# Optimization experiments

Hardware: AMD Instinct MI355X
Metric: run time of the kernel (lower is better)

## Reference

```python
import jax, jax.numpy as jnp
import numpy as np

B, O, D = 64, 36, 512
G1, G2 = 512, 512  # interactor sizes
F1, F2 = 512, 512  # aggregator sizes
BN_EPS = 1e-5


def setup_inputs() -> dict:
    key = jax.random.key(0)
    ks = jax.random.split(key, 10)
    sc = 0.02
    return {
        "objs": jax.random.normal(ks[0], (B, O, D), jnp.float32),
        "W1": jax.random.normal(ks[1], (G1, 2 * D), jnp.float32) * sc,
        "b1": jax.random.normal(ks[2], (G1,), jnp.float32) * sc,
        "W2": jax.random.normal(ks[3], (G2, G1), jnp.float32) * sc,
        "b2": jax.random.normal(ks[4], (G2,), jnp.float32) * sc,
        "gamma": jnp.ones((G2,), jnp.float32),
        "beta": jnp.zeros((G2,), jnp.float32),
        "W3": jax.random.normal(ks[5], (F1, G2), jnp.float32) * sc,
        "b3": jax.random.normal(ks[6], (F1,), jnp.float32) * sc,
        "W4": jax.random.normal(ks[7], (F2, F1), jnp.float32) * sc,
        "b4": jax.random.normal(ks[8], (F2,), jnp.float32) * sc,
    }


def reference(objs, W1, b1, W2, b2, gamma, beta, W3, b3, W4, b4):
    b, o, d = objs.shape
    # make_pairs: x_full[b,k,m] = concat(v[b,m], v[b,k]) -> (b, o*o, 2d)
    v_i = jnp.broadcast_to(objs[:, None, :, :], (b, o, o, d))  # varies over m
    v_j = jnp.broadcast_to(objs[:, :, None, :], (b, o, o, d))  # varies over k
    pairs = jnp.concatenate([v_i, v_j], axis=-1).reshape(b, o * o, 2 * d)
    # interaction MLP g
    h = jax.nn.relu(jnp.einsum('bpc,gc->bpg', pairs, W1) + b1)
    x_pairs = jax.nn.relu(jnp.einsum('bpg,hg->bph', h, W2) + b2)
    # sum over pairs, BatchNorm1d (training mode: batch stats, biased var)
    s = x_pairs.sum(axis=1)  # (b, G2)
    mean = s.mean(axis=0)
    var = ((s - mean) ** 2).mean(axis=0)
    sn = (s - mean) / jnp.sqrt(var + BN_EPS) * gamma + beta
    # aggregation MLP f
    a = jax.nn.relu(sn @ W3.T + b3)
    agg = jax.nn.relu(a @ W4.T + b4)
    return agg, x_pairs
```

## Files before the change

### kernel.cpp

```cpp
#include <hip/hip_runtime.h>
#include <cstdint>
#include <cstddef>

#define B_  64
#define O_  36
#define D_  512
#define P_  (O_*O_)
#define BO_ (B_*O_)

typedef short s8v __attribute__((ext_vector_type(8)));
typedef float f4v __attribute__((ext_vector_type(4)));

__device__ __forceinline__ void bsplit(float x, short& hi, short& lo) {
    unsigned u = __float_as_uint(x);
    unsigned r = (u + 0x7FFFu + ((u >> 16) & 1u)) >> 16;
    hi = (short)r;
    float hf = __uint_as_float(r << 16);
    float d = x - hf;
    unsigned u2 = __float_as_uint(d);
    unsigned r2 = (u2 + 0x7FFFu + ((u2 >> 16) & 1u)) >> 16;
    lo = (short)r2;
}

__global__ __launch_bounds__(256) void wsplit_all(
    const float* __restrict__ W2, const float* __restrict__ W1,
    short* __restrict__ W2h, short* __restrict__ W2l,
    short* __restrict__ W1h, short* __restrict__ W1l)
{
    int i = (blockIdx.x * 256 + threadIdx.x) * 4;
    float4 w;
    short* hip_; short* lop_; int o;
    if (i < 512 * 512) {
        w = *(const float4*)&W2[i];
        hip_ = W2h; lop_ = W2l; o = i;
    } else {
        o = i - 512 * 512;
        const int n = o >> 9, d = o & 511;
        w = *(const float4*)&W1[(size_t)(n & 511) * 1024 + ((n >> 9) << 9) + d];
        hip_ = W1h; lop_ = W1l;
    }
    short h0, l0, h1, l1, h2, l2, h3, l3;
    bsplit(w.x, h0, l0); bsplit(w.y, h1, l1);
    bsplit(w.z, h2, l2); bsplit(w.w, h3, l3);
    *(short4*)&hip_[o] = make_short4(h0, h1, h2, h3);
    *(short4*)&lop_[o] = make_short4(l0, l1, l2, l3);
}

__global__ __launch_bounds__(256, 2) void uv_mfma(
    const float* __restrict__ objs,
    const short* __restrict__ W1h, const short* __restrict__ W1l,
    float* __restrict__ U, float* __restrict__ V)
{
    __shared__ short Ah[128 * 40];
    __shared__ short Al[128 * 40];
    __shared__ short Bh[128 * 40];
    __shared__ short Bl[128 * 40];

    const int tid  = threadIdx.x;
    const int lane = tid & 63;
    const int wid  = tid >> 6;
    const int wr   = wid >> 1, wc = wid & 1;
    const int rowbase = blockIdx.y * 128;
    const int colbase = blockIdx.x * 128;

    const int srow = tid >> 1;
    const int skq  = (tid & 1) * 8;
    const float* Xrow  = objs + (size_t)(rowbase + srow) * 512;
    const short* Whrow = W1h + (size_t)(colbase + srow) * 512;
    const short* Wlrow = W1l + (size_t)(colbase + srow) * 512;

    const int fr = lane & 15;
    const int sl = (lane >> 4) * 8;
    const int abase = (wr * 64 + fr) * 40 + sl;
    const int bbase = (wc * 64 + fr) * 40 + sl;

    f4v acc[4][4];
    const f4v zero = {0.f, 0.f, 0.f, 0.f};
    #pragma unroll
    for (int i = 0; i < 4; ++i)
        #pragma unroll
        for (int j = 0; j < 4; ++j) acc[i][j] = zero;

    for (int kt = 0; kt < 512; kt += 32) {
        __syncthreads();
        #pragma unroll
        for (int pass = 0; pass < 2; ++pass) {
            const int kq = skq + pass * 16;
            const float4 x0 = *(const float4*)&Xrow[kt + kq];
            const float4 x1 = *(const float4*)&Xrow[kt + kq + 4];
            float hx[8] = {x0.x, x0.y, x0.z, x0.w, x1.x, x1.y, x1.z, x1.w};
            s8v hi8, lo8;
            #pragma unroll
            for (int j = 0; j < 8; ++j) { short h, l; bsplit(hx[j], h, l); hi8[j] = h; lo8[j] = l; }
            *(s8v*)&Ah[srow * 40 + kq] = hi8;
            *(s8v*)&Al[srow * 40 + kq] = lo8;
            *(s8v*)&Bh[srow * 40 + kq] = *(const s8v*)&Whrow[kt + kq];
            *(s8v*)&Bl[srow * 40 + kq] = *(const s8v*)&Wlrow[kt + kq];
        }
        __syncthreads();

        s8v ah[4], al[4], bh[4], bl[4];
        #pragma unroll
        for (int f = 0; f < 4; ++f) {
            ah[f] = *(const s8v*)&Ah[abase + f * 640];
            al[f] = *(const s8v*)&Al[abase + f * 640];
            bh[f] = *(const s8v*)&Bh[bbase + f * 640];
            bl[f] = *(const s8v*)&Bl[bbase + f * 640];
        }
        #pragma unroll
        for (int fm = 0; fm < 4; ++fm)
            #pragma unroll
            for (int fn = 0; fn < 4; ++fn)
                acc[fm][fn] = __builtin_amdgcn_mfma_f32_16x16x32_bf16(ah[fm], bh[fn], acc[fm][fn], 0, 0, 0);
        #pragma unroll
        for (int fm = 0; fm < 4; ++fm)
            #pragma unroll
            for (int fn = 0; fn < 4; ++fn)
                acc[fm][fn] = __builtin_amdgcn_mfma_f32_16x16x32_bf16(ah[fm], bl[fn], acc[fm][fn], 0, 0, 0);
        #pragma unroll
        for (int fm = 0; fm < 4; ++fm)
            #pragma unroll
            for (int fn = 0; fn < 4; ++fn)
                acc[fm][fn] = __builtin_amdgcn_mfma_f32_16x16x32_bf16(al[fm], bh[fn], acc[fm][fn], 0, 0, 0);
    }

    float* dst = (colbase < 512) ? U : V;
    const int cb = colbase & 511;
    const int r4 = (lane >> 4) * 4;
    #pragma unroll
    for (int fm = 0; fm < 4; ++fm) {
        #pragma unroll
        for (int r = 0; r < 4; ++r) {
            const int row = rowbase + wr * 64 + fm * 16 + r4 + r;
            float* drow = &dst[(size_t)row * 512 + cb + wc * 64 + fr];
            #pragma unroll
            for (int fn = 0; fn < 4; ++fn) drow[fn * 16] = acc[fm][fn][r];
        }
    }
}

__global__ __launch_bounds__(256, 3) void pair_gemm(
    const float* __restrict__ U, const float* __restrict__ V,
    const float* __restrict__ b1,
    const short* __restrict__ W2h, const short* __restrict__ W2l,
    const float* __restrict__ b2,
    float* __restrict__ xout, float* __restrict__ s)
{
    __shared__ short Ah[4][128][8];
    __shared__ short Al[4][128][8];
    __shared__ short Bh[4][128][8];
    __shared__ short Bl[4][128][8];
    __shared__ float b1s[512];

    const int tid  = threadIdx.x;
    const int lane = tid & 63;
    const int wid  = tid >> 6;
    const int wr   = wid >> 1, wc = wid & 1;
    const int b       = blockIdx.z;
    const int pbase   = blockIdx.y * 128;
    const int colbase = blockIdx.x * 128;

    for (int g = tid; g < 512; g += 256) b1s[g] = b1[g];

    const int arow = tid & 127;
    const int a0   = (tid >> 7) * 2;
    const int p    = pbase + arow;
    const bool valid = (p < P_);
    int ki = 0, mi = 0;
    if (valid) { ki = p / O_; mi = p - ki * O_; }
    const float* Urow = U + (size_t)(b * O_ + mi) * 512;
    const float* Vrow = V + (size_t)(b * O_ + ki) * 512;

    const int boct = wid;
    const int brow = lane;
    const short* Wh0 = W2h + (size_t)(colbase + brow) * 512 + boct * 8;
    const short* Wh1 = Wh0 + (size_t)64 * 512;
    const short* Wl0 = W2l + (size_t)(colbase + brow) * 512 + boct * 8;
    const short* Wl1 = Wl0 + (size_t)64 * 512;

    const int fr = lane & 15;
    const int q  = lane >> 4;

    f4v acc[4][4];
    const f4v zero = {0.f, 0.f, 0.f, 0.f};
    #pragma unroll
    for (int i = 0; i < 4; ++i)
        #pragma unroll
        for (int j = 0; j < 4; ++j) acc[i][j] = zero;

    for (int kt = 0; kt < 512; kt += 32) {
        __syncthreads();
        const s8v wh0 = *(const s8v*)&Wh0[kt];
        const s8v wh1 = *(const s8v*)&Wh1[kt];
        const s8v wl0 = *(const s8v*)&Wl0[kt];
        const s8v wl1 = *(const s8v*)&Wl1[kt];
        #pragma unroll
        for (int j = 0; j < 2; ++j) {
            const int oct = a0 + j;
            const int k0  = kt + oct * 8;
            s8v hi8, lo8;
            if (valid) {
                const float4 u0 = *(const float4*)&Urow[k0];
                const float4 u1 = *(const float4*)&Urow[k0 + 4];
                const float4 v0 = *(const float4*)&Vrow[k0];
                const float4 v1 = *(const float4*)&Vrow[k0 + 4];
                const float4 c0 = *(const float4*)&b1s[k0];
                const float4 c1 = *(const float4*)&b1s[k0 + 4];
                float hx[8];
                hx[0] = fmaxf(u0.x + v0.x + c0.x, 0.f);
                hx[1] = fmaxf(u0.y + v0.y + c0.y, 0.f);
                hx[2] = fmaxf(u0.z + v0.z + c0.z, 0.f);
                hx[3] = fmaxf(u0.w + v0.w + c0.w, 0.f);
                hx[4] = fmaxf(u1.x + v1.x + c1.x, 0.f);
                hx[5] = fmaxf(u1.y + v1.y + c1.y, 0.f);
                hx[6] = fmaxf(u1.z + v1.z + c1.z, 0.f);
                hx[7] = fmaxf(u1.w + v1.w + c1.w, 0.f);
                #pragma unroll
                for (int e = 0; e < 8; ++e) { short h, l; bsplit(hx[e], h, l); hi8[e] = h; lo8[e] = l; }
            } else {
                #pragma unroll
                for (int e = 0; e < 8; ++e) { hi8[e] = 0; lo8[e] = 0; }
            }
            *(s8v*)&Ah[oct][arow][0] = hi8;
            *(s8v*)&Al[oct][arow][0] = lo8;
        }
        *(s8v*)&Bh[boct][brow][0]      = wh0;
        *(s8v*)&Bh[boct][64 + brow][0] = wh1;
        *(s8v*)&Bl[boct][brow][0]      = wl0;
        *(s8v*)&Bl[boct][64 + brow][0] = wl1;
        __syncthreads();

        s8v ah[4], al[4], bh[4], bl[4];
        #pragma unroll
        for (int f = 0; f < 4; ++f) {
            ah[f] = *(const s8v*)&Ah[q][wr * 64 + f * 16 + fr][0];
            al[f] = *(const s8v*)&Al[q][wr * 64 + f * 16 + fr][0];
            bh[f] = *(const s8v*)&Bh[q][wc * 64 + f * 16 + fr][0];
            bl[f] = *(const s8v*)&Bl[q][wc * 64 + f * 16 + fr][0];
        }
        #pragma unroll
        for (int fm = 0; fm < 4; ++fm)
            #pragma unroll
            for (int fn = 0; fn < 4; ++fn)
                acc[fm][fn] = __builtin_amdgcn_mfma_f32_16x16x32_bf16(ah[fm], bh[fn], acc[fm][fn], 0, 0, 0);
        #pragma unroll
        for (int fm = 0; fm < 4; ++fm)
            #pragma unroll
            for (int fn = 0; fn < 4; ++fn)
                acc[fm][fn] = __builtin_amdgcn_mfma_f32_16x16x32_bf16(ah[fm], bl[fn], acc[fm][fn], 0, 0, 0);
        #pragma unroll
        for (int fm = 0; fm < 4; ++fm)
            #pragma unroll
            for (int fn = 0; fn < 4; ++fn)
                acc[fm][fn] = __builtin_amdgcn_mfma_f32_16x16x32_bf16(al[fm], bh[fn], acc[fm][fn], 0, 0, 0);
    }

    float b2v[4];
    #pragma unroll
    for (int fn = 0; fn < 4; ++fn) b2v[fn] = b2[colbase + wc * 64 + fn * 16 + fr];
    const int r4 = (lane >> 4) * 4;
    float csum[4] = {0.f, 0.f, 0.f, 0.f};
    #pragma unroll
    for (int fm = 0; fm < 4; ++fm) {
        const int prow0 = pbase + wr * 64 + fm * 16 + r4;
        #pragma unroll
        for (int r = 0; r < 4; ++r) {
            const int pp = prow0 + r;
            if (pp < P_) {
                float* xrow = &xout[(size_t)(b * P_ + pp) * 512 + colbase + wc * 64 + fr];
                #pragma unroll
                for (int fn = 0; fn < 4; ++fn) {
                    float x = fmaxf(acc[fm][fn][r] + b2v[fn], 0.f);
                    xrow[fn * 16] = x;
                    csum[fn] += x;
                }
            }
        }
    }
    #pragma unroll
    for (int fn = 0; fn < 4; ++fn) {
        csum[fn] += __shfl_xor(csum[fn], 16);
        csum[fn] += __shfl_xor(csum[fn], 32);
    }
    if (lane < 16) {
        #pragma unroll
        for (int fn = 0; fn < 4; ++fn)
            atomicAdd(&s[b * 512 + colbase + wc * 64 + fn * 16 + lane], csum[fn]);
    }
}

__global__ __launch_bounds__(512) void bn_kernel(
    const float* __restrict__ s, const float* __restrict__ gamma,
    const float* __restrict__ beta, float* __restrict__ sn)
{
    const int g = threadIdx.x;
    float mean = 0.f;
    for (int b = 0; b < B_; ++b) mean += s[b * 512 + g];
    mean *= (1.f / B_);
    float var = 0.f;
    for (int b = 0; b < B_; ++b) { const float d = s[b * 512 + g] - mean; var = fmaf(d, d, var); }
    var *= (1.f / B_);
    const float inv = 1.f / sqrtf(var + 1e-5f);
    const float ga = gamma[g], be = beta[g];
    for (int b = 0; b < B_; ++b)
        sn[b * 512 + g] = (s[b * 512 + g] - mean) * inv * ga + be;
}

__global__ __launch_bounds__(256) void mlp512(
    const float* __restrict__ x, const float* __restrict__ W,
    const float* __restrict__ bias, float* __restrict__ out)
{
    __shared__ float xs[512];
    const int b = blockIdx.y;
    const int f = blockIdx.x * 256 + threadIdx.x;
    for (int g = threadIdx.x; g < 512; g += 256) xs[g] = x[b * 512 + g];
    __syncthreads();
    float sum = 0.f;
    #pragma unroll 8
    for (int k = 0; k < 512; k += 4) {
        const float4 w4 = *(const float4*)&W[(size_t)f * 512 + k];
        const float4 x4 = *(const float4*)&xs[k];
        sum = fmaf(w4.x, x4.x, sum); sum = fmaf(w4.y, x4.y, sum);
        sum = fmaf(w4.z, x4.z, sum); sum = fmaf(w4.w, x4.w, sum);
    }
    out[b * 512 + f] = fmaxf(sum + bias[f], 0.f);
}

extern "C" void kernel_launch(void* const* d_in, const int* in_sizes, int n_in,
                              void* d_out, int out_size, void* d_ws, size_t ws_size,
                              hipStream_t stream)
{
    const float* objs  = (const float*)d_in[0];
    const float* W1    = (const float*)d_in[1];
    const float* b1    = (const float*)d_in[2];
    const float* W2    = (const float*)d_in[3];
    const float* b2    = (const float*)d_in[4];
    const float* gamma = (const float*)d_in[5];
    const float* beta  = (const float*)d_in[6];
    const float* W3    = (const float*)d_in[7];
    const float* b3    = (const float*)d_in[8];
    const float* W4    = (const float*)d_in[9];
    const float* b4    = (const float*)d_in[10];

    float* out  = (float*)d_out;
    float* xout = out + B_ * 512;

    float* U  = (float*)d_ws;
    float* V  = U  + (size_t)BO_ * 512;
    float* s  = V  + (size_t)BO_ * 512;
    float* sn = s  + B_ * 512;
    float* a  = sn + B_ * 512;
    short* W2h = (short*)(a + B_ * 512);
    short* W2l = W2h + (size_t)512 * 512;
    short* W1h = W2l + (size_t)512 * 512;
    short* W1l = W1h + (size_t)1024 * 512;

    wsplit_all<<<768, 256, 0, stream>>>(W2, W1, W2h, W2l, W1h, W1l);
    uv_mfma<<<dim3(8, 18), 256, 0, stream>>>(objs, W1h, W1l, U, V);
    hipMemsetAsync(s, 0, B_ * 512 * sizeof(float), stream);
    pair_gemm<<<dim3(4, 11, B_), 256, 0, stream>>>(U, V, b1, W2h, W2l, b2, xout, s);
    bn_kernel<<<1, 512, 0, stream>>>(s, gamma, beta, sn);
    mlp512<<<dim3(2, B_), 256, 0, stream>>>(sn, W3, b3, a);
    mlp512<<<dim3(2, B_), 256, 0, stream>>>(a, W4, b4, out);
}
```

Before: 451.3 us.

## Double-buffer pair GEMM, load W2 fragments directly, fuse MLPs and memset

```diff
diff --git a/kernel.cpp b/kernel.cpp
--- a/kernel.cpp
+++ b/kernel.cpp
@@ -25,9 +25,13 @@
 __global__ __launch_bounds__(256) void wsplit_all(
     const float* __restrict__ W2, const float* __restrict__ W1,
     short* __restrict__ W2h, short* __restrict__ W2l,
-    short* __restrict__ W1h, short* __restrict__ W1l)
-{
-    int i = (blockIdx.x * 256 + threadIdx.x) * 4;
+    short* __restrict__ W1h, short* __restrict__ W1l,
+    float* __restrict__ s)
+{
+    const int gt = blockIdx.x * 256 + threadIdx.x;
+    if (gt < 8192)
+        *(float4*)&s[gt * 4] = make_float4(0.f, 0.f, 0.f, 0.f);
+    int i = gt * 4;
     float4 w;
     short* hip_; short* lop_; int o;
     if (i < 512 * 512) {
@@ -139,17 +143,15 @@
     }
 }
 
-__global__ __launch_bounds__(256, 3) void pair_gemm(
+__global__ __launch_bounds__(256, 2) void pair_gemm(
     const float* __restrict__ U, const float* __restrict__ V,
     const float* __restrict__ b1,
     const short* __restrict__ W2h, const short* __restrict__ W2l,
     const float* __restrict__ b2,
     float* __restrict__ xout, float* __restrict__ s)
 {
-    __shared__ short Ah[4][128][8];
-    __shared__ short Al[4][128][8];
-    __shared__ short Bh[4][128][8];
-    __shared__ short Bl[4][128][8];
+    __shared__ short Ah[2][4][128][8];
+    __shared__ short Al[2][4][128][8];
     __shared__ float b1s[512];
 
     const int tid  = threadIdx.x;
@@ -171,16 +173,70 @@
     const float* Urow = U + (size_t)(b * O_ + mi) * 512;
     const float* Vrow = V + (size_t)(b * O_ + ki) * 512;
 
-    const int boct = wid;
-    const int brow = lane;
-    const short* Wh0 = W2h + (size_t)(colbase + brow) * 512 + boct * 8;
-    const short* Wh1 = Wh0 + (size_t)64 * 512;
-    const short* Wl0 = W2l + (size_t)(colbase + brow) * 512 + boct * 8;
-    const short* Wl1 = Wl0 + (size_t)64 * 512;
-
     const int fr = lane & 15;
     const int q  = lane >> 4;
 
+    const short* Bhp[4]; const short* Blp[4];
+    #pragma unroll
+    for (int f = 0; f < 4; ++f) {
+        const size_t off = (size_t)(colbase + wc * 64 + f * 16 + fr) * 512 + q * 8;
+        Bhp[f] = W2h + off; Blp[f] = W2l + off;
+    }
+
+    float4 au0[2], au1[2], av0[2], av1[2];
+    s8v bhA[4], blA[4], bhB[4], blB[4];
+    s8v ah[4], al[4];
+
+#define LOAD_A(ktv) do { if (valid) { const int _k = (ktv); \
+    _Pragma("unroll") for (int _j = 0; _j < 2; ++_j) { \
+        const int _o = _k + (a0 + _j) * 8; \
+        au0[_j] = *(const float4*)&Urow[_o]; au1[_j] = *(const float4*)&Urow[_o + 4]; \
+        av0[_j] = *(const float4*)&Vrow[_o]; av1[_j] = *(const float4*)&Vrow[_o + 4]; } } } while (0)
+
+#define BUILD_WRITE(bufi, ktv) do { const int _k = (ktv); \
+    _Pragma("unroll") for (int _j = 0; _j < 2; ++_j) { \
+        const int _oct = a0 + _j; \
+        s8v _hi, _lo; \
+        if (valid) { \
+            const float4 _c0 = *(const float4*)&b1s[_k + _oct * 8]; \
+            const float4 _c1 = *(const float4*)&b1s[_k + _oct * 8 + 4]; \
+            float _hx[8]; \
+            _hx[0] = fmaxf(au0[_j].x + av0[_j].x + _c0.x, 0.f); \
+            _hx[1] = fmaxf(au0[_j].y + av0[_j].y + _c0.y, 0.f); \
+            _hx[2] = fmaxf(au0[_j].z + av0[_j].z + _c0.z, 0.f); \
+            _hx[3] = fmaxf(au0[_j].w + av0[_j].w + _c0.w, 0.f); \
+            _hx[4] = fmaxf(au1[_j].x + av1[_j].x + _c1.x, 0.f); \
+            _hx[5] = fmaxf(au1[_j].y + av1[_j].y + _c1.y, 0.f); \
+            _hx[6] = fmaxf(au1[_j].z + av1[_j].z + _c1.z, 0.f); \
+            _hx[7] = fmaxf(au1[_j].w + av1[_j].w + _c1.w, 0.f); \
+            _Pragma("unroll") for (int _e = 0; _e < 8; ++_e) { short _h, _l; bsplit(_hx[_e], _h, _l); _hi[_e] = _h; _lo[_e] = _l; } \
+        } else { \
+            _Pragma("unroll") for (int _e = 0; _e < 8; ++_e) { _hi[_e] = 0; _lo[_e] = 0; } \
+        } \
+        *(s8v*)&Ah[bufi][_oct][arow][0] = _hi; \
+        *(s8v*)&Al[bufi][_oct][arow][0] = _lo; } } while (0)
+
+#define LOAD_B(ktv, BH, BL) do { const int _k = (ktv); \
+    _Pragma("unroll") for (int _f = 0; _f < 4; ++_f) { \
+        BH[_f] = *(const s8v*)&Bhp[_f][_k]; BL[_f] = *(const s8v*)&Blp[_f][_k]; } } while (0)
+
+#define READ_FRAGS(bufi) do { \
+    _Pragma("unroll") for (int _f = 0; _f < 4; ++_f) { \
+        ah[_f] = *(const s8v*)&Ah[bufi][q][wr * 64 + _f * 16 + fr][0]; \
+        al[_f] = *(const s8v*)&Al[bufi][q][wr * 64 + _f * 16 + fr][0]; } } while (0)
+
+#define MFMA_STEP(BH, BL) do { \
+    _Pragma("unroll") for (int _fm = 0; _fm < 4; ++_fm) \
+        _Pragma("unroll") for (int _fn = 0; _fn < 4; ++_fn) \
+            acc[_fm][_fn] = __builtin_amdgcn_mfma_f32_16x16x32_bf16(ah[_fm], BH[_fn], acc[_fm][_fn], 0, 0, 0); \
+    _Pragma("unroll") for (int _fm = 0; _fm < 4; ++_fm) \
+        _Pragma("unroll") for (int _fn = 0; _fn < 4; ++_fn) \
+            acc[_fm][_fn] = __builtin_amdgcn_mfma_f32_16x16x32_bf16(ah[_fm], BL[_fn], acc[_fm][_fn], 0, 0, 0); \
+    _Pragma("unroll") for (int _fm = 0; _fm < 4; ++_fm) \
+        _Pragma("unroll") for (int _fn = 0; _fn < 4; ++_fn) \
+            acc[_fm][_fn] = __builtin_amdgcn_mfma_f32_16x16x32_bf16(al[_fm], BH[_fn], acc[_fm][_fn], 0, 0, 0); \
+    } while (0)
+
     f4v acc[4][4];
     const f4v zero = {0.f, 0.f, 0.f, 0.f};
     #pragma unroll
@@ -188,71 +244,28 @@
         #pragma unroll
         for (int j = 0; j < 4; ++j) acc[i][j] = zero;
 
-    for (int kt = 0; kt < 512; kt += 32) {
+    LOAD_A(0);
+    __syncthreads();
+    BUILD_WRITE(0, 0);
+    LOAD_A(32);
+    LOAD_B(0, bhA, blA);
+
+    for (int it = 0; it < 8; ++it) {
+        const int kt0 = it * 64;
         __syncthreads();
-        const s8v wh0 = *(const s8v*)&Wh0[kt];
-        const s8v wh1 = *(const s8v*)&Wh1[kt];
-        const s8v wl0 = *(const s8v*)&Wl0[kt];
-        const s8v wl1 = *(const s8v*)&Wl1[kt];
-        #pragma unroll
-        for (int j = 0; j < 2; ++j) {
-            const int oct = a0 + j;
-            const int k0  = kt + oct * 8;
-            s8v hi8, lo8;
-            if (valid) {
-                const float4 u0 = *(const float4*)&Urow[k0];
-                const float4 u1 = *(const float4*)&Urow[k0 + 4];
-                const float4 v0 = *(const float4*)&Vrow[k0];
-                const float4 v1 = *(const float4*)&Vrow[k0 + 4];
-                const float4 c0 = *(const float4*)&b1s[k0];
-                const float4 c1 = *(const float4*)&b1s[k0 + 4];
-                float hx[8];
-                hx[0] = fmaxf(u0.x + v0.x + c0.x, 0.f);
-                hx[1] = fmaxf(u0.y + v0.y + c0.y, 0.f);
-                hx[2] = fmaxf(u0.z + v0.z + c0.z, 0.f);
-                hx[3] = fmaxf(u0.w + v0.w + c0.w, 0.f);
-                hx[4] = fmaxf(u1.x + v1.x + c1.x, 0.f);
-                hx[5] = fmaxf(u1.y + v1.y + c1.y, 0.f);
-                hx[6] = fmaxf(u1.z + v1.z + c1.z, 0.f);
-                hx[7] = fmaxf(u1.w + v1.w + c1.w, 0.f);
-                #pragma unroll
-                for (int e = 0; e < 8; ++e) { short h, l; bsplit(hx[e], h, l); hi8[e] = h; lo8[e] = l; }
-            } else {
-                #pragma unroll
-                for (int e = 0; e < 8; ++e) { hi8[e] = 0; lo8[e] = 0; }
-            }
-            *(s8v*)&Ah[oct][arow][0] = hi8;
-            *(s8v*)&Al[oct][arow][0] = lo8;
-        }
-        *(s8v*)&Bh[boct][brow][0]      = wh0;
-        *(s8v*)&Bh[boct][64 + brow][0] = wh1;
-        *(s8v*)&Bl[boct][brow][0]      = wl0;
-        *(s8v*)&Bl[boct][64 + brow][0] = wl1;
+        READ_FRAGS(0);
+        LOAD_B(kt0 + 32, bhB, blB);
+        MFMA_STEP(bhA, blA);
+        BUILD_WRITE(1, kt0 + 32);
+        LOAD_A(kt0 + 64 > 480 ? 480 : kt0 + 64);
         __syncthreads();
-
-        s8v ah[4], al[4], bh[4], bl[4];
-        #pragma unroll
-        for (int f = 0; f < 4; ++f) {
-            ah[f] = *(const s8v*)&Ah[q][wr * 64 + f * 16 + fr][0];
-            al[f] = *(const s8v*)&Al[q][wr * 64 + f * 16 + fr][0];
-            bh[f] = *(const s8v*)&Bh[q][wc * 64 + f * 16 + fr][0];
-            bl[f] = *(const s8v*)&Bl[q][wc * 64 + f * 16 + fr][0];
-        }
-        #pragma unroll
-        for (int fm = 0; fm < 4; ++fm)
-            #pragma unroll
-            for (int fn = 0; fn < 4; ++fn)
-                acc[fm][fn] = __builtin_amdgcn_mfma_f32_16x16x32_bf16(ah[fm], bh[fn], acc[fm][fn], 0, 0, 0);
-        #pragma unroll
-        for (int fm = 0; fm < 4; ++fm)
-            #pragma unroll
-            for (int fn = 0; fn < 4; ++fn)
-                acc[fm][fn] = __builtin_amdgcn_mfma_f32_16x16x32_bf16(ah[fm], bl[fn], acc[fm][fn], 0, 0, 0);
-        #pragma unroll
-        for (int fm = 0; fm < 4; ++fm)
-            #pragma unroll
-            for (int fn = 0; fn < 4; ++fn)
-                acc[fm][fn] = __builtin_amdgcn_mfma_f32_16x16x32_bf16(al[fm], bh[fn], acc[fm][fn], 0, 0, 0);
+        READ_FRAGS(1);
+        LOAD_B(kt0 + 64 > 480 ? 480 : kt0 + 64, bhA, blA);
+        MFMA_STEP(bhB, blB);
+        if (it < 7) {
+            BUILD_WRITE(0, kt0 + 64);
+            LOAD_A(kt0 + 96 > 480 ? 480 : kt0 + 96);
+        }
     }
 
     float b2v[4];
@@ -287,6 +300,11 @@
         for (int fn = 0; fn < 4; ++fn)
             atomicAdd(&s[b * 512 + colbase + wc * 64 + fn * 16 + lane], csum[fn]);
     }
+#undef LOAD_A
+#undef BUILD_WRITE
+#undef LOAD_B
+#undef READ_FRAGS
+#undef MFMA_STEP
 }
 
 __global__ __launch_bounds__(512) void bn_kernel(
@@ -294,36 +312,55 @@
     const float* __restrict__ beta, float* __restrict__ sn)
 {
     const int g = threadIdx.x;
+    float v[64];
+    #pragma unroll
+    for (int b = 0; b < 64; ++b) v[b] = s[b * 512 + g];
     float mean = 0.f;
-    for (int b = 0; b < B_; ++b) mean += s[b * 512 + g];
+    #pragma unroll
+    for (int b = 0; b < 64; ++b) mean += v[b];
     mean *= (1.f / B_);
     float var = 0.f;
-    for (int b = 0; b < B_; ++b) { const float d = s[b * 512 + g] - mean; var = fmaf(d, d, var); }
+    #pragma unroll
+    for (int b = 0; b < 64; ++b) { const float d = v[b] - mean; var = fmaf(d, d, var); }
     var *= (1.f / B_);
     const float inv = 1.f / sqrtf(var + 1e-5f);
     const float ga = gamma[g], be = beta[g];
-    for (int b = 0; b < B_; ++b)
-        sn[b * 512 + g] = (s[b * 512 + g] - mean) * inv * ga + be;
-}
-
-__global__ __launch_bounds__(256) void mlp512(
-    const float* __restrict__ x, const float* __restrict__ W,
-    const float* __restrict__ bias, float* __restrict__ out)
+    #pragma unroll
+    for (int b = 0; b < 64; ++b)
+        sn[b * 512 + g] = (v[b] - mean) * inv * ga + be;
+}
+
+__global__ __launch_bounds__(512) void mlp_fused(
+    const float* __restrict__ sn,
+    const float* __restrict__ W3, const float* __restrict__ b3,
+    const float* __restrict__ W4, const float* __restrict__ b4,
+    float* __restrict__ out)
 {
     __shared__ float xs[512];
-    const int b = blockIdx.y;
-    const int f = blockIdx.x * 256 + threadIdx.x;
-    for (int g = threadIdx.x; g < 512; g += 256) xs[g] = x[b * 512 + g];
+    __shared__ float as_[512];
+    const int b = blockIdx.x;
+    const int f = threadIdx.x;
+    xs[f] = sn[b * 512 + f];
     __syncthreads();
     float sum = 0.f;
     #pragma unroll 8
     for (int k = 0; k < 512; k += 4) {
-        const float4 w4 = *(const float4*)&W[(size_t)f * 512 + k];
+        const float4 w4 = *(const float4*)&W3[(size_t)f * 512 + k];
         const float4 x4 = *(const float4*)&xs[k];
         sum = fmaf(w4.x, x4.x, sum); sum = fmaf(w4.y, x4.y, sum);
         sum = fmaf(w4.z, x4.z, sum); sum = fmaf(w4.w, x4.w, sum);
     }
-    out[b * 512 + f] = fmaxf(sum + bias[f], 0.f);
+    as_[f] = fmaxf(sum + b3[f], 0.f);
+    __syncthreads();
+    float sum2 = 0.f;
+    #pragma unroll 8
+    for (int k = 0; k < 512; k += 4) {
+        const float4 w4 = *(const float4*)&W4[(size_t)f * 512 + k];
+        const float4 x4 = *(const float4*)&as_[k];
+        sum2 = fmaf(w4.x, x4.x, sum2); sum2 = fmaf(w4.y, x4.y, sum2);
+        sum2 = fmaf(w4.z, x4.z, sum2); sum2 = fmaf(w4.w, x4.w, sum2);
+    }
+    out[b * 512 + f] = fmaxf(sum2 + b4[f], 0.f);
 }
 
 extern "C" void kernel_launch(void* const* d_in, const int* in_sizes, int n_in,
@@ -349,17 +386,14 @@
     float* V  = U  + (size_t)BO_ * 512;
     float* s  = V  + (size_t)BO_ * 512;
     float* sn = s  + B_ * 512;
-    float* a  = sn + B_ * 512;
-    short* W2h = (short*)(a + B_ * 512);
+    short* W2h = (short*)(sn + B_ * 512);
     short* W2l = W2h + (size_t)512 * 512;
     short* W1h = W2l + (size_t)512 * 512;
     short* W1l = W1h + (size_t)1024 * 512;
 
-    wsplit_all<<<768, 256, 0, stream>>>(W2, W1, W2h, W2l, W1h, W1l);
+    wsplit_all<<<768, 256, 0, stream>>>(W2, W1, W2h, W2l, W1h, W1l, s);
     uv_mfma<<<dim3(8, 18), 256, 0, stream>>>(objs, W1h, W1l, U, V);
-    hipMemsetAsync(s, 0, B_ * 512 * sizeof(float), stream);
     pair_gemm<<<dim3(4, 11, B_), 256, 0, stream>>>(U, V, b1, W2h, W2l, b2, xout, s);
     bn_kernel<<<1, 512, 0, stream>>>(s, gamma, beta, sn);
-    mlp512<<<dim3(2, B_), 256, 0, stream>>>(sn, W3, b3, a);
-    mlp512<<<dim3(2, B_), 256, 0, stream>>>(a, W4, b4, out);
-}
+    mlp_fused<<<B_, 512, 0, stream>>>(sn, W3, b3, W4, b4, out);
+}
```

After: 572.0 us. 26.7% more time.
